# Kernel tuning notes

Measured on AMD Instinct MI355X. Metric: run time of the kernel, lower is better.

## Reference

```python
import jax, jax.numpy as jnp
import numpy as np

TOP_K = 2
HORIZON = 10


def _lstm_layer(seq, w_ih, w_hh, b_ih, b_hh):
    """Single torch-style LSTM layer over seq [T, in]; returns hidden seq [T, hid]."""
    hid = w_hh.shape[1]
    def step(carry, x_t):
        h, c = carry
        z = x_t @ w_ih.T + h @ w_hh.T + b_ih + b_hh  # [4*hid], torch gate order i,f,g,o
        i, f, g, o = jnp.split(z, 4)
        c = jax.nn.sigmoid(f) * c + jax.nn.sigmoid(i) * jnp.tanh(g)
        h = jax.nn.sigmoid(o) * jnp.tanh(c)
        return (h, c), h
    init = (jnp.zeros((hid,), seq.dtype), jnp.zeros((hid,), seq.dtype))
    _, hs = jax.lax.scan(step, init, seq)
    return hs


def setup_inputs() -> dict:
    key = jax.random.key(0)
    ks = jax.random.split(key, 12)
    H, E = 4096, 64
    B, S = 4, 4096
    s = 0.02
    return {
        "x": jax.random.normal(ks[0], (B, S, H), jnp.float32),
        "gate_w": jax.random.normal(ks[1], (E, H), jnp.float32) * s,
        "expert_bias": jnp.zeros((E,), jnp.float32),
        "cp_w1": jax.random.normal(ks[2], (64, H), jnp.float32) * s,
        "cp_b1": jnp.zeros((64,), jnp.float32),
        "cp_w2": jax.random.normal(ks[3], (1, 64), jnp.float32) * s,
        "cp_b2": jnp.zeros((1,), jnp.float32),
        "load_buffer": jax.random.uniform(ks[4], (50, E), jnp.float32),
        "lp_w_ih0": jax.random.normal(ks[5], (256, E), jnp.float32) * s,
        "lp_w_hh0": jax.random.normal(ks[6], (256, 64), jnp.float32) * s,
        "lp_b_ih0": jnp.zeros((256,), jnp.float32),
        "lp_b_hh0": jnp.zeros((256,), jnp.float32),
        "lp_w_ih1": jax.random.normal(ks[7], (256, 64), jnp.float32) * s,
        "lp_w_hh1": jax.random.normal(ks[8], (256, 64), jnp.float32) * s,
        "lp_b_ih1": jnp.zeros((256,), jnp.float32),
        "lp_b_hh1": jnp.zeros((256,), jnp.float32),
        "head_w": jax.random.normal(ks[9], (E * HORIZON, 64), jnp.float32) * s,
        "head_b": jnp.zeros((E * HORIZON,), jnp.float32),
    }


def reference(x, gate_w, expert_bias, cp_w1, cp_b1, cp_w2, cp_b2, load_buffer,
              lp_w_ih0, lp_w_hh0, lp_b_ih0, lp_b_hh0,
              lp_w_ih1, lp_w_hh1, lp_b_ih1, lp_b_hh1, head_w, head_b):
    sg = jax.lax.stop_gradient
    B, S, H = x.shape
    E = gate_w.shape[0]
    flat = x.reshape(-1, H)                       # [N, H]
    N = flat.shape[0]

    # --- routing logits (small gate GEMM) ---
    logits = flat @ gate_w.T                      # [N, E]

    # --- LSTM load prediction (torch.no_grad in original) ---
    seq = sg(load_buffer)
    h1 = _lstm_layer(seq, sg(lp_w_ih0), sg(lp_w_hh0), sg(lp_b_ih0), sg(lp_b_hh0))
    h2 = _lstm_layer(h1, sg(lp_w_ih1), sg(lp_w_hh1), sg(lp_b_ih1), sg(lp_b_hh1))
    pred = h2[-1] @ sg(head_w).T + sg(head_b)     # [E*HORIZON]
    future_load = jax.nn.softmax(pred.reshape(E, HORIZON).mean(axis=1))  # [E]

    # --- bias + predicted-load adjustment, softmax, top-k ---
    adj_logits = logits + expert_bias - sg(future_load)
    probs = jax.nn.softmax(adj_logits, axis=-1)   # [N, E]
    top_scores, top_idx = jax.lax.top_k(probs, TOP_K)
    top_scores = top_scores / top_scores.sum(axis=-1, keepdims=True)

    # --- switch-style load-balancing auxiliary loss ---
    one_hot = jax.nn.one_hot(top_idx, E, dtype=probs.dtype)   # [N, k, E]
    f = one_hot.sum(axis=(0, 1)) / (N * TOP_K)                # routed fraction per expert
    P = probs.mean(axis=0)                                    # mean routing prob
    aux_loss = E * jnp.sum(f * P)

    # --- dynamic capacity from complexity predictor (torch.no_grad) ---
    comp = jax.nn.sigmoid(
        jax.nn.relu(flat @ sg(cp_w1).T + sg(cp_b1)) @ sg(cp_w2).T + sg(cp_b2))  # [N,1]
    capacity = jnp.clip(0.5 + 1.5 * comp.mean(), 0.5, 2.0)

    return top_scores, top_idx, aux_loss, capacity, future_load
```

## Files before the change

kernel.cpp:

```cpp
#include <hip/hip_runtime.h>
#include <stdint.h>

#define IMG_OFF_BYTES 80000
#define CHUNK_IMG 16384
#define LOGITS_OFF 680000
#define SLAB 2097152
#define TAU 1e-3f

#define XLOFF 5120
#define BUF_STRIDE 10240

typedef __attribute__((ext_vector_type(8))) short short8v;
typedef __attribute__((ext_vector_type(4))) short short4v;
typedef __attribute__((ext_vector_type(4))) float f32x4;

__device__ __forceinline__ float rlf(float v, int l) {
  return __int_as_float(__builtin_amdgcn_readlane(__float_as_int(v), l));
}
__device__ __forceinline__ float wsum(float v) {
#pragma unroll
  for (int o = 32; o; o >>= 1) v += __shfl_xor(v, o, 64);
  return v;
}
__device__ __forceinline__ float wmax(float v) {
#pragma unroll
  for (int o = 32; o; o >>= 1) v = fmaxf(v, __shfl_xor(v, o, 64));
  return v;
}
__device__ __forceinline__ unsigned short f2bf(float f) {
  unsigned u = __float_as_uint(f);
  u += 0x7fffu + ((u >> 16) & 1u);
  return (unsigned short)(u >> 16);
}
__device__ __forceinline__ float bf2f(unsigned short h) {
  return __uint_as_float(((unsigned)h) << 16);
}
__device__ __forceinline__ short8v frag8(const char* p0, const char* p1) {
  short4v a = *(const short4v*)p0;
  short4v b = *(const short4v*)p1;
  return __builtin_shufflevector(a, b, 0, 1, 2, 3, 4, 5, 6, 7);
}

__device__ __forceinline__ void lds_barrier() {
  asm volatile("s_waitcnt lgkmcnt(0)" ::: "memory");
  __builtin_amdgcn_s_barrier();
  asm volatile("" ::: "memory");
  __builtin_amdgcn_sched_barrier(0);
}

__global__ __launch_bounds__(256) void prep_kernel(
    const float* __restrict__ gate_w, const float* __restrict__ cp_w1,
    float* __restrict__ ws)
{
  const int c = blockIdx.x;
  const int tid = threadIdx.x;
  if (c == 0 && tid < 144) ws[64 + tid] = 0.f;
  const int row = tid >> 1;
  const int half = tid & 1;
  const float* src = ((row < 64) ? (gate_w + (size_t)row * 4096)
                                 : (cp_w1 + (size_t)(row - 64) * 4096)) + c * 32 + half * 16;
  float v[16];
#pragma unroll
  for (int j = 0; j < 4; ++j) *(float4*)&v[j * 4] = *(const float4*)(src + j * 4);
  const int g = row >> 4, r15 = row & 15;
  char* img = (char*)ws + IMG_OFF_BYTES + (size_t)c * CHUNK_IMG + g * 2048;
#pragma unroll
  for (int q = 0; q < 4; ++q) {
    unsigned short h0 = f2bf(v[4 * q + 0]), h1 = f2bf(v[4 * q + 1]);
    unsigned short h2 = f2bf(v[4 * q + 2]), h3 = f2bf(v[4 * q + 3]);
    unsigned short l0 = f2bf(v[4 * q + 0] - bf2f(h0));
    unsigned short l1 = f2bf(v[4 * q + 1] - bf2f(h1));
    unsigned short l2 = f2bf(v[4 * q + 2] - bf2f(h2));
    unsigned short l3 = f2bf(v[4 * q + 3] - bf2f(h3));
    uint2 hv, lv;
    hv.x = (unsigned)h0 | ((unsigned)h1 << 16);
    hv.y = (unsigned)h2 | ((unsigned)h3 << 16);
    lv.x = (unsigned)l0 | ((unsigned)l1 << 16);
    lv.y = (unsigned)l2 | ((unsigned)l3 << 16);
    const int l = q * 16 + r15;
    *(uint2*)(img + l * 16 + half * 8) = hv;
    *(uint2*)(img + 1024 + l * 16 + half * 8) = lv;
  }
}

__device__ void lstm_device(
    char* ldsbase,
    const float* __restrict__ lb,
    const float* __restrict__ wih0, const float* __restrict__ whh0,
    const float* __restrict__ bih0, const float* __restrict__ bhh0,
    const float* __restrict__ wih1, const float* __restrict__ whh1,
    const float* __restrict__ bih1, const float* __restrict__ bhh1,
    const float* __restrict__ head_w, const float* __restrict__ head_b,
    float* __restrict__ ws, float* __restrict__ out, int N)
{
  float* seqh = (float*)ldsbase;
  float* h1s  = seqh + 3200;
  float* zbuf = h1s + 3200;
  float* hbuf = zbuf + 256;
  float* preds = hbuf + 64;
  const int tid = threadIdx.x;
  const int lane = tid & 63;
  for (int i = tid; i < 3200; i += 256) seqh[i] = lb[i];

  float hv = 0.f;
#pragma unroll 1
  for (int L = 0; L < 2; ++L) {
    const float* wip  = L ? wih1 : wih0;
    const float* whp  = L ? whh1 : whh0;
    const float* bip  = L ? bih1 : bih0;
    const float* bhp  = L ? bhh1 : bhh0;
    const float* seqp = L ? h1s  : seqh;
    float wiR[64], whR[64];
#pragma unroll
    for (int j = 0; j < 64; j += 4) {
      *(float4*)&wiR[j] = *(const float4*)(wip + tid * 64 + j);
      *(float4*)&whR[j] = *(const float4*)(whp + tid * 64 + j);
    }
    const float bsum = bip[tid] + bhp[tid];
    float c_reg = 0.f;
    hv = 0.f;
    if (tid < 64) hbuf[tid] = 0.f;
    __syncthreads();
#pragma unroll 1
    for (int t = 0; t < 50; ++t) {
      const float xv = seqp[t * 64 + lane];
      float a0 = bsum, a1 = 0.f, a2 = 0.f, a3 = 0.f;
#pragma unroll
      for (int j = 0; j < 64; j += 4) {
        a0 = fmaf(rlf(xv, j + 0), wiR[j + 0], a0);
        a1 = fmaf(rlf(xv, j + 1), wiR[j + 1], a1);
        a2 = fmaf(rlf(xv, j + 2), wiR[j + 2], a2);
        a3 = fmaf(rlf(xv, j + 3), wiR[j + 3], a3);
      }
#pragma unroll
      for (int j = 0; j < 64; j += 4) {
        a0 = fmaf(rlf(hv, j + 0), whR[j + 0], a0);
        a1 = fmaf(rlf(hv, j + 1), whR[j + 1], a1);
        a2 = fmaf(rlf(hv, j + 2), whR[j + 2], a2);
        a3 = fmaf(rlf(hv, j + 3), whR[j + 3], a3);
      }
      zbuf[tid] = (a0 + a1) + (a2 + a3);
      __syncthreads();
      if (tid < 64) {
        const float zi = zbuf[tid], zf = zbuf[64 + tid];
        const float zg = zbuf[128 + tid], zo = zbuf[192 + tid];
        const float si = 1.f / (1.f + expf(-zi));
        const float sf = 1.f / (1.f + expf(-zf));
        const float so = 1.f / (1.f + expf(-zo));
        c_reg = sf * c_reg + si * tanhf(zg);
        const float h = so * tanhf(c_reg);
        hbuf[tid] = h;
        if (L == 0) h1s[t * 64 + tid] = h;
      }
      __syncthreads();
      hv = hbuf[lane];
    }
    __syncthreads();
  }
  for (int o = tid; o < 640; o += 256) {
    const float* hw = head_w + o * 64;
    float a0 = 0.f, a1 = 0.f, a2 = 0.f, a3 = 0.f;
#pragma unroll
    for (int j = 0; j < 64; j += 4) {
      a0 = fmaf(rlf(hv, j + 0), hw[j + 0], a0);
      a1 = fmaf(rlf(hv, j + 1), hw[j + 1], a1);
      a2 = fmaf(rlf(hv, j + 2), hw[j + 2], a2);
      a3 = fmaf(rlf(hv, j + 3), hw[j + 3], a3);
    }
    preds[o] = (a0 + a1) + (a2 + a3) + head_b[o];
  }
  __syncthreads();
  if (tid < 64) {
    float m = 0.f;
#pragma unroll
    for (int h = 0; h < 10; ++h) m += preds[tid * 10 + h];
    m = m / 10.f;
    const float mx = wmax(m);
    const float p = expf(m - mx);
    const float s = wsum(p);
    const float flv = p / s;
    ws[tid] = flv;
    out[4 * N + 2 + tid] = flv;
  }
}

__global__ __launch_bounds__(256) void gemm_kernel(
    const float* __restrict__ x, float* __restrict__ ws, float* __restrict__ out,
    const float* __restrict__ lb,
    const float* __restrict__ wih0, const float* __restrict__ whh0,
    const float* __restrict__ bih0, const float* __restrict__ bhh0,
    const float* __restrict__ wih1, const float* __restrict__ whh1,
    const float* __restrict__ bih1, const float* __restrict__ bhh1,
    const float* __restrict__ head_w, const float* __restrict__ head_b,
    int N)
{
  __shared__ __align__(16) char lds[34048];
  if (blockIdx.x == 0) {
    lstm_device(lds, lb, wih0, whh0, bih0, bhh0, wih1, whh1, bih1, bhh1,
                head_w, head_b, ws, out, N);
    return;
  }
  const int b = blockIdx.x - 1;
  const int tb = (b & 255) * 64;
  const int kq = b >> 8;
  const int ck0 = kq * 32;
  const int tid = threadIdx.x;
  const int lane = tid & 63;
  const int wv = __builtin_amdgcn_readfirstlane(tid >> 6);
  const int r15 = lane & 15;
  const int fo = (lane >> 4) * 8;
  const int row = tid >> 2;
  const int kslot = tid & 3;
  const float* xsrc = x + (size_t)(tb + row) * 4096 + kslot * 8;
  const char* wimg = (const char*)ws + IMG_OFF_BYTES;
  char* buf0 = lds;
  char* buf1 = lds + BUF_STRIDE;

  f32x4 acc[4][2];
#pragma unroll
  for (int mi = 0; mi < 4; ++mi)
#pragma unroll
    for (int ni = 0; ni < 2; ++ni) acc[mi][ni] = (f32x4)0.f;

  float xa[8], xb[8];
  short8v whA[2], wlA[2], whB[2], wlB[2];

#define LOADX(R, C)                                                        \
  { *(float4*)&R[0] = *(const float4*)(xsrc + (size_t)(C) * 32);           \
    *(float4*)&R[4] = *(const float4*)(xsrc + (size_t)(C) * 32 + 4); }

#define WRITEX(R, BASE)                                                    \
  { uint4 hv, lv; unsigned hu[4], lu[4];                                   \
    _Pragma("unroll")                                                      \
    for (int i = 0; i < 4; ++i) {                                          \
      unsigned short h0 = f2bf(R[2 * i]), h1 = f2bf(R[2 * i + 1]);         \
      unsigned short l0 = f2bf(R[2 * i] - bf2f(h0));                       \
      unsigned short l1 = f2bf(R[2 * i + 1] - bf2f(h1));                   \
      hu[i] = (unsigned)h0 | ((unsigned)h1 << 16);                         \
      lu[i] = (unsigned)l0 | ((unsigned)l1 << 16);                         \
    }                                                                      \
    hv.x = hu[0]; hv.y = hu[1]; hv.z = hu[2]; hv.w = hu[3];                \
    lv.x = lu[0]; lv.y = lu[1]; lv.z = lu[2]; lv.w = lu[3];                \
    *(uint4*)((BASE) + row * 80 + kslot * 16) = hv;                        \
    *(uint4*)((BASE) + XLOFF + row * 80 + kslot * 16) = lv; }

#define WLOADR(C, WH, WL)                                                  \
  { const char* wb = wimg + (size_t)(C) * CHUNK_IMG + wv * 4096 + lane * 16; \
    WH[0] = *(const short8v*)wb;                                           \
    WL[0] = *(const short8v*)(wb + 1024);                                  \
    WH[1] = *(const short8v*)(wb + 2048);                                  \
    WL[1] = *(const short8v*)(wb + 3072); }

#define COMPUTE(BASE, WH, WL)                                              \
  { short8v xh[4], xl[4];                                                  \
    _Pragma("unroll")                                                      \
    for (int mi = 0; mi < 4; ++mi) {                                       \
      const char* p = (BASE) + (mi * 16 + r15) * 80 + fo;                  \
      xh[mi] = frag8(p, p + 32);                                           \
      xl[mi] = frag8(p + XLOFF, p + XLOFF + 32);                           \
    }                                                                      \
    _Pragma("unroll")                                                      \
    for (int mi = 0; mi < 4; ++mi)                                         \
      _Pragma("unroll")                                                    \
      for (int ni = 0; ni < 2; ++ni) {                                     \
        acc[mi][ni] = __builtin_amdgcn_mfma_f32_16x16x32_bf16(             \
            xh[mi], WH[ni], acc[mi][ni], 0, 0, 0);                         \
        acc[mi][ni] = __builtin_amdgcn_mfma_f32_16x16x32_bf16(             \
            xh[mi], WL[ni], acc[mi][ni], 0, 0, 0);                         \
        acc[mi][ni] = __builtin_amdgcn_mfma_f32_16x16x32_bf16(             \
            xl[mi], WH[ni], acc[mi][ni], 0, 0, 0);                         \
      } }

  LOADX(xa, ck0);
  LOADX(xb, ck0 + 1);
  WLOADR(ck0, whA, wlA);
  WRITEX(xa, buf0);
  lds_barrier();

#pragma unroll 1
  for (int cc = 0; cc < 16; ++cc) {
    const int c0 = ck0 + 2 * cc, c1 = c0 + 1;
    WLOADR(c1, whB, wlB);
    if (cc < 15) LOADX(xa, c0 + 2);
    COMPUTE(buf0, whA, wlA);
    WRITEX(xb, buf1);
    lds_barrier();
    if (cc < 15) WLOADR(c0 + 2, whA, wlA);
    if (cc < 15) LOADX(xb, c1 + 2);
    COMPUTE(buf1, whB, wlB);
    if (cc < 15) WRITEX(xa, buf0);
    lds_barrier();
  }

  float (*souts)[132] = (float(*)[132])lds;
#pragma unroll
  for (int mi = 0; mi < 4; ++mi)
#pragma unroll
    for (int ni = 0; ni < 2; ++ni)
#pragma unroll
      for (int r = 0; r < 4; ++r)
        souts[mi * 16 + (lane >> 4) * 4 + r][wv * 32 + ni * 16 + r15] =
            acc[mi][ni][r];
  lds_barrier();
  {
    float* slab = ws + LOGITS_OFF + (size_t)kq * SLAB;
    const int srow = tid >> 2, sq = tid & 3;
    float4* dst = (float4*)(slab + (size_t)(tb + srow) * 128 + sq * 32);
    const float4* srcp = (const float4*)&souts[srow][sq * 32];
#pragma unroll
    for (int i = 0; i < 8; ++i) dst[i] = srcp[i];
  }
#undef LOADX
#undef WRITEX
#undef WLOADR
#undef COMPUTE
}

__global__ __launch_bounds__(256) void epi_kernel(
    const float* __restrict__ eb_p, const float* __restrict__ cp_b1,
    const float* __restrict__ cp_w2, const float* __restrict__ cp_b2,
    float* __restrict__ ws, float* __restrict__ out, int N)
{
  const int tid = threadIdx.x;
  const int lane = tid & 63;
  const int wv = __builtin_amdgcn_readfirstlane(tid >> 6);
  const int tb = blockIdx.x * 32;
  const float* lg = ws + LOGITS_OFF;
  int* qd = (int*)(ws + 200);
  __shared__ float sP[64];
  __shared__ float scnt[64];
  __shared__ float scomp;
  if (tid < 64) { sP[tid] = 0.f; scnt[tid] = 0.f; }
  if (tid == 0) scomp = 0.f;
  __syncthreads();

  const float eb = eb_p[lane];
  const float fl = ws[lane];
  const float cb1 = cp_b1[lane];
  const float cw2 = cp_w2[lane];
  const float cb2 = cp_b2[0];
  float psum_local = 0.f, comp_local = 0.f;
  float* o_ts = out;
  float* o_ti = out + 2 * N;

#pragma unroll 1
  for (int tt = 0; tt < 8; ++tt) {
    const int tok = tb + wv * 8 + tt;
    const size_t base = (size_t)tok * 128;
    const float lgv = ((lg[base + lane] + lg[SLAB + base + lane]) +
                       (lg[2 * SLAB + base + lane] + lg[3 * SLAB + base + lane]));
    const float lc  = ((lg[base + 64 + lane] + lg[SLAB + base + 64 + lane]) +
                       (lg[2 * SLAB + base + 64 + lane] + lg[3 * SLAB + base + 64 + lane]));
    float rr = fmaxf(lc + cb1, 0.f) * cw2;
    rr = wsum(rr);
    const float comp = 1.f / (1.f + expf(-(rr + cb2)));
    comp_local += comp;
    const float a = lgv + eb - fl;
    float m1 = a; int i1 = lane;
#pragma unroll
    for (int o = 32; o; o >>= 1) {
      const float ov = __shfl_xor(m1, o, 64);
      const int oi = __shfl_xor(i1, o, 64);
      if (ov > m1 || (ov == m1 && oi < i1)) { m1 = ov; i1 = oi; }
    }
    float m2 = (lane == i1) ? -1e30f : a; int i2 = lane;
#pragma unroll
    for (int o = 32; o; o >>= 1) {
      const float ov = __shfl_xor(m2, o, 64);
      const int oi = __shfl_xor(i2, o, 64);
      if (ov > m2 || (ov == m2 && oi < i2)) { m2 = ov; i2 = oi; }
    }
    float m3 = (lane == i1 || lane == i2) ? -1e30f : a;
#pragma unroll
    for (int o = 32; o; o >>= 1) m3 = fmaxf(m3, __shfl_xor(m3, o, 64));
    const float p = expf(a - m1);
    const float ssum = wsum(p);
    const float prob = p / ssum;
    psum_local += prob;
    const float s1 = rlf(prob, i1);
    const float s2 = rlf(prob, i2);
    if (lane == 0) {
      const float inv = 1.f / (s1 + s2);
      o_ts[tok * 2 + 0] = s1 * inv;
      o_ts[tok * 2 + 1] = s2 * inv;
      o_ti[tok * 2 + 0] = (float)i1;
      o_ti[tok * 2 + 1] = (float)i2;
      atomicAdd(&scnt[i1], 1.f);
      atomicAdd(&scnt[i2], 1.f);
      if (m1 - m2 < TAU || m2 - m3 < TAU) {
        int slot = atomicAdd(qd, 1);
        qd[8 + slot] = tok;
      }
    }
  }
  atomicAdd(&sP[lane], psum_local);
  if (lane == 0) atomicAdd(&scomp, comp_local);
  __syncthreads();
  if (tid < 64) {
    atomicAdd(&ws[64 + tid], sP[tid]);
    atomicAdd(&ws[128 + tid], scnt[tid]);
  }
  if (tid == 0) atomicAdd(&ws[192], scomp);
}

__global__ __launch_bounds__(256) void repair_kernel(
    const float* __restrict__ x, const float* __restrict__ gate_w,
    const float* __restrict__ eb_p, float* __restrict__ ws,
    float* __restrict__ out, int N)
{
  const int tid = threadIdx.x;
  __shared__ float red[256];
  int* qd = (int*)(ws + 200);
  const int qn = qd[0];
  float* o_ts = out;
  float* o_ti = out + 2 * N;

  for (int e = blockIdx.x; e < qn; e += gridDim.x) {
    const int tok = qd[8 + e];
    const int o = tid & 63;
    const int kq = tid >> 6;
    const float* xr = x + (size_t)tok * 4096 + kq * 1024;
    const float* wr = gate_w + (size_t)o * 4096 + kq * 1024;
    float s = 0.f;
#pragma unroll 4
    for (int j = 0; j < 256; ++j) {
      const float4 xv = *(const float4*)(xr + j * 4);
      const float4 wv = *(const float4*)(wr + j * 4);
      s = fmaf(xv.x, wv.x, s); s = fmaf(xv.y, wv.y, s);
      s = fmaf(xv.z, wv.z, s); s = fmaf(xv.w, wv.w, s);
    }
    red[tid] = s;
    __syncthreads();
    if (tid < 64) {
      const float a = red[tid] + red[64 + tid] + red[128 + tid] +
                      red[192 + tid] + eb_p[tid] - ws[tid];
      const int lane = tid;
      float m1 = a; int i1 = lane;
#pragma unroll
      for (int oo = 32; oo; oo >>= 1) {
        const float ov = __shfl_xor(m1, oo, 64);
        const int oi = __shfl_xor(i1, oo, 64);
        if (ov > m1 || (ov == m1 && oi < i1)) { m1 = ov; i1 = oi; }
      }
      float m2 = (lane == i1) ? -1e30f : a; int i2 = lane;
#pragma unroll
      for (int oo = 32; oo; oo >>= 1) {
        const float ov = __shfl_xor(m2, oo, 64);
        const int oi = __shfl_xor(i2, oo, 64);
        if (ov > m2 || (ov == m2 && oi < i2)) { m2 = ov; i2 = oi; }
      }
      const float p = expf(a - m1);
      const float ssum = wsum(p);
      const float s1 = rlf(p, i1) / ssum;
      const float s2 = rlf(p, i2) / ssum;
      if (lane == 0) {
        const int i1o = (int)o_ti[tok * 2 + 0];
        const int i2o = (int)o_ti[tok * 2 + 1];
        const float inv = 1.f / (s1 + s2);
        o_ts[tok * 2 + 0] = s1 * inv;
        o_ts[tok * 2 + 1] = s2 * inv;
        o_ti[tok * 2 + 0] = (float)i1;
        o_ti[tok * 2 + 1] = (float)i2;
        if (i1o != i1 || i2o != i2) {
          atomicAdd(&ws[128 + i1o], -1.f);
          atomicAdd(&ws[128 + i2o], -1.f);
          atomicAdd(&ws[128 + i1], 1.f);
          atomicAdd(&ws[128 + i2], 1.f);
        }
      }
    }
    __syncthreads();
  }
}

__global__ __launch_bounds__(64) void fin_kernel(const float* __restrict__ ws,
                                                 float* __restrict__ out, int N) {
  const int e = threadIdx.x;
  const float P = ws[64 + e] / (float)N;
  const float f = ws[128 + e] / (float)(2 * N);
  const float v = wsum(f * P);
  if (e == 0) {
    out[4 * N + 0] = 64.f * v;
    float cap = 0.5f + 1.5f * (ws[192] / (float)N);
    out[4 * N + 1] = fminf(fmaxf(cap, 0.5f), 2.f);
  }
}

extern "C" void kernel_launch(void* const* d_in, const int* in_sizes, int n_in,
                              void* d_out, int out_size, void* d_ws, size_t ws_size,
                              hipStream_t stream) {
  const float* x          = (const float*)d_in[0];
  const float* gate_w     = (const float*)d_in[1];
  const float* expert_bias= (const float*)d_in[2];
  const float* cp_w1      = (const float*)d_in[3];
  const float* cp_b1      = (const float*)d_in[4];
  const float* cp_w2      = (const float*)d_in[5];
  const float* cp_b2      = (const float*)d_in[6];
  const float* load_buffer= (const float*)d_in[7];
  const float* wih0       = (const float*)d_in[8];
  const float* whh0       = (const float*)d_in[9];
  const float* bih0       = (const float*)d_in[10];
  const float* bhh0       = (const float*)d_in[11];
  const float* wih1       = (const float*)d_in[12];
  const float* whh1       = (const float*)d_in[13];
  const float* bih1       = (const float*)d_in[14];
  const float* bhh1       = (const float*)d_in[15];
  const float* head_w     = (const float*)d_in[16];
  const float* head_b     = (const float*)d_in[17];
  float* out = (float*)d_out;
  float* ws  = (float*)d_ws;
  const int N = in_sizes[0] / 4096;

  prep_kernel<<<128, 256, 0, stream>>>(gate_w, cp_w1, ws);
  gemm_kernel<<<1025, 256, 0, stream>>>(x, ws, out, load_buffer,
                                        wih0, whh0, bih0, bhh0,
                                        wih1, whh1, bih1, bhh1,
                                        head_w, head_b, N);
  epi_kernel<<<N / 32, 256, 0, stream>>>(expert_bias, cp_b1, cp_w2, cp_b2,
                                         ws, out, N);
  repair_kernel<<<128, 256, 0, stream>>>(x, gate_w, expert_bias, ws, out, N);
  fin_kernel<<<1, 64, 0, stream>>>(ws, out, N);
}
```

Measured before the change: 216.6 us.

## Load x straight into registers as MFMA fragments, dropping LDS staging and barriers

The GEMM kernel no longer stages x through double-buffered LDS with barriers. Each wave now loads its own 32 token rows directly from global memory into registers and splits them into bf16 hi/lo MFMA operands in place. Weight fragments are streamed from the prepacked image one group at a time, interleaved with the MFMAs. Tiles grow to 128 tokens per block with half as many blocks, and results are stored straight to the logits slab without an LDS transpose. This removes LDS traffic and synchronisation, but increases register pressure (16 accumulators) and each wave now reloads the weights on its own.

Result: slower. 287.7 us (+32.8%).

```diff
diff --git a/kernel.cpp b/kernel.cpp
--- a/kernel.cpp
+++ b/kernel.cpp
@@ -7,12 +7,9 @@
 #define SLAB 2097152
 #define TAU 1e-3f
 
-#define XLOFF 5120
-#define BUF_STRIDE 10240
-
 typedef __attribute__((ext_vector_type(8))) short short8v;
-typedef __attribute__((ext_vector_type(4))) short short4v;
 typedef __attribute__((ext_vector_type(4))) float f32x4;
+typedef unsigned short ushort;
 
 __device__ __forceinline__ float rlf(float v, int l) {
   return __int_as_float(__builtin_amdgcn_readlane(__float_as_int(v), l));
@@ -27,25 +24,30 @@
   for (int o = 32; o; o >>= 1) v = fmaxf(v, __shfl_xor(v, o, 64));
   return v;
 }
-__device__ __forceinline__ unsigned short f2bf(float f) {
+__device__ __forceinline__ ushort f2bf(float f) {
   unsigned u = __float_as_uint(f);
   u += 0x7fffu + ((u >> 16) & 1u);
-  return (unsigned short)(u >> 16);
-}
-__device__ __forceinline__ float bf2f(unsigned short h) {
+  return (ushort)(u >> 16);
+}
+__device__ __forceinline__ float bf2f(ushort h) {
   return __uint_as_float(((unsigned)h) << 16);
 }
-__device__ __forceinline__ short8v frag8(const char* p0, const char* p1) {
-  short4v a = *(const short4v*)p0;
-  short4v b = *(const short4v*)p1;
-  return __builtin_shufflevector(a, b, 0, 1, 2, 3, 4, 5, 6, 7);
-}
-
-__device__ __forceinline__ void lds_barrier() {
-  asm volatile("s_waitcnt lgkmcnt(0)" ::: "memory");
-  __builtin_amdgcn_s_barrier();
-  asm volatile("" ::: "memory");
-  __builtin_amdgcn_sched_barrier(0);
+
+__device__ __forceinline__ void split8(const float4 a, const float4 b,
+                                       short8v& hv, short8v& lv) {
+  union { ushort u[8]; short8v v; } H, L;
+  const float f[8] = {a.x, a.y, a.z, a.w, b.x, b.y, b.z, b.w};
+#pragma unroll
+  for (int i = 0; i < 8; ++i) {
+    unsigned u = __float_as_uint(f[i]);
+    unsigned t = u + 0x7fffu + ((u >> 16) & 1u);
+    H.u[i] = (ushort)(t >> 16);
+    const float e = f[i] - __uint_as_float(t & 0xffff0000u);
+    unsigned ue = __float_as_uint(e);
+    unsigned te = ue + 0x7fffu + ((ue >> 16) & 1u);
+    L.u[i] = (ushort)(te >> 16);
+  }
+  hv = H.v; lv = L.v;
 }
 
 __global__ __launch_bounds__(256) void prep_kernel(
@@ -66,12 +68,12 @@
   char* img = (char*)ws + IMG_OFF_BYTES + (size_t)c * CHUNK_IMG + g * 2048;
 #pragma unroll
   for (int q = 0; q < 4; ++q) {
-    unsigned short h0 = f2bf(v[4 * q + 0]), h1 = f2bf(v[4 * q + 1]);
-    unsigned short h2 = f2bf(v[4 * q + 2]), h3 = f2bf(v[4 * q + 3]);
-    unsigned short l0 = f2bf(v[4 * q + 0] - bf2f(h0));
-    unsigned short l1 = f2bf(v[4 * q + 1] - bf2f(h1));
-    unsigned short l2 = f2bf(v[4 * q + 2] - bf2f(h2));
-    unsigned short l3 = f2bf(v[4 * q + 3] - bf2f(h3));
+    ushort h0 = f2bf(v[4 * q + 0]), h1 = f2bf(v[4 * q + 1]);
+    ushort h2 = f2bf(v[4 * q + 2]), h3 = f2bf(v[4 * q + 3]);
+    ushort l0 = f2bf(v[4 * q + 0] - bf2f(h0));
+    ushort l1 = f2bf(v[4 * q + 1] - bf2f(h1));
+    ushort l2 = f2bf(v[4 * q + 2] - bf2f(h2));
+    ushort l3 = f2bf(v[4 * q + 3] - bf2f(h3));
     uint2 hv, lv;
     hv.x = (unsigned)h0 | ((unsigned)h1 << 16);
     hv.y = (unsigned)h2 | ((unsigned)h3 << 16);
@@ -194,126 +196,96 @@
     const float* __restrict__ head_w, const float* __restrict__ head_b,
     int N)
 {
-  __shared__ __align__(16) char lds[34048];
+  __shared__ __align__(16) char lds[29440];
   if (blockIdx.x == 0) {
     lstm_device(lds, lb, wih0, whh0, bih0, bhh0, wih1, whh1, bih1, bhh1,
                 head_w, head_b, ws, out, N);
     return;
   }
   const int b = blockIdx.x - 1;
-  const int tb = (b & 255) * 64;
-  const int kq = b >> 8;
+  const int tile = (b & 127) * 128;
+  const int kq = b >> 7;
   const int ck0 = kq * 32;
-  const int tid = threadIdx.x;
-  const int lane = tid & 63;
-  const int wv = __builtin_amdgcn_readfirstlane(tid >> 6);
+  const int lane = threadIdx.x & 63;
+  const int wv = __builtin_amdgcn_readfirstlane(threadIdx.x >> 6);
   const int r15 = lane & 15;
-  const int fo = (lane >> 4) * 8;
-  const int row = tid >> 2;
-  const int kslot = tid & 3;
-  const float* xsrc = x + (size_t)(tb + row) * 4096 + kslot * 8;
+  const int q = lane >> 4;
+
+  const float* xs0 = x + (size_t)(tile + wv * 32 + r15) * 4096 + ck0 * 32 + q * 4;
+  const float* xs1 = xs0 + (size_t)16 * 4096;
   const char* wimg = (const char*)ws + IMG_OFF_BYTES;
-  char* buf0 = lds;
-  char* buf1 = lds + BUF_STRIDE;
-
-  f32x4 acc[4][2];
-#pragma unroll
-  for (int mi = 0; mi < 4; ++mi)
-#pragma unroll
-    for (int ni = 0; ni < 2; ++ni) acc[mi][ni] = (f32x4)0.f;
-
-  float xa[8], xb[8];
-  short8v whA[2], wlA[2], whB[2], wlB[2];
-
-#define LOADX(R, C)                                                        \
-  { *(float4*)&R[0] = *(const float4*)(xsrc + (size_t)(C) * 32);           \
-    *(float4*)&R[4] = *(const float4*)(xsrc + (size_t)(C) * 32 + 4); }
-
-#define WRITEX(R, BASE)                                                    \
-  { uint4 hv, lv; unsigned hu[4], lu[4];                                   \
-    _Pragma("unroll")                                                      \
-    for (int i = 0; i < 4; ++i) {                                          \
-      unsigned short h0 = f2bf(R[2 * i]), h1 = f2bf(R[2 * i + 1]);         \
-      unsigned short l0 = f2bf(R[2 * i] - bf2f(h0));                       \
-      unsigned short l1 = f2bf(R[2 * i + 1] - bf2f(h1));                   \
-      hu[i] = (unsigned)h0 | ((unsigned)h1 << 16);                         \
-      lu[i] = (unsigned)l0 | ((unsigned)l1 << 16);                         \
-    }                                                                      \
-    hv.x = hu[0]; hv.y = hu[1]; hv.z = hu[2]; hv.w = hu[3];                \
-    lv.x = lu[0]; lv.y = lu[1]; lv.z = lu[2]; lv.w = lu[3];                \
-    *(uint4*)((BASE) + row * 80 + kslot * 16) = hv;                        \
-    *(uint4*)((BASE) + XLOFF + row * 80 + kslot * 16) = lv; }
-
-#define WLOADR(C, WH, WL)                                                  \
-  { const char* wb = wimg + (size_t)(C) * CHUNK_IMG + wv * 4096 + lane * 16; \
-    WH[0] = *(const short8v*)wb;                                           \
-    WL[0] = *(const short8v*)(wb + 1024);                                  \
-    WH[1] = *(const short8v*)(wb + 2048);                                  \
-    WL[1] = *(const short8v*)(wb + 3072); }
-
-#define COMPUTE(BASE, WH, WL)                                              \
-  { short8v xh[4], xl[4];                                                  \
-    _Pragma("unroll")                                                      \
-    for (int mi = 0; mi < 4; ++mi) {                                       \
-      const char* p = (BASE) + (mi * 16 + r15) * 80 + fo;                  \
-      xh[mi] = frag8(p, p + 32);                                           \
-      xl[mi] = frag8(p + XLOFF, p + XLOFF + 32);                           \
-    }                                                                      \
-    _Pragma("unroll")                                                      \
-    for (int mi = 0; mi < 4; ++mi)                                         \
-      _Pragma("unroll")                                                    \
-      for (int ni = 0; ni < 2; ++ni) {                                     \
-        acc[mi][ni] = __builtin_amdgcn_mfma_f32_16x16x32_bf16(             \
-            xh[mi], WH[ni], acc[mi][ni], 0, 0, 0);                         \
-        acc[mi][ni] = __builtin_amdgcn_mfma_f32_16x16x32_bf16(             \
-            xh[mi], WL[ni], acc[mi][ni], 0, 0, 0);                         \
-        acc[mi][ni] = __builtin_amdgcn_mfma_f32_16x16x32_bf16(             \
-            xl[mi], WH[ni], acc[mi][ni], 0, 0, 0);                         \
-      } }
-
-  LOADX(xa, ck0);
-  LOADX(xb, ck0 + 1);
-  WLOADR(ck0, whA, wlA);
-  WRITEX(xa, buf0);
-  lds_barrier();
+
+  f32x4 acc[8][2];
+#pragma unroll
+  for (int g = 0; g < 8; ++g)
+#pragma unroll
+    for (int s = 0; s < 2; ++s) acc[g][s] = (f32x4)0.f;
+
+  float4 raE[2], rbE[2], raO[2], rbO[2];
+  short8v xh[2], xl[2];
+  short8v whA, wlA, whB, wlB;
+
+#define LX(RA, RB, RC)                                                      \
+  { RA[0] = *(const float4*)(xs0 + (RC) * 32);                              \
+    RB[0] = *(const float4*)(xs0 + (RC) * 32 + 16);                         \
+    RA[1] = *(const float4*)(xs1 + (RC) * 32);                              \
+    RB[1] = *(const float4*)(xs1 + (RC) * 32 + 16); }
+
+#define WG(RC, G, WH, WL)                                                   \
+  { const char* p_ = wimg + (size_t)((ck0 + (RC)) & 127) * CHUNK_IMG +      \
+                     (G) * 2048 + lane * 16;                                \
+    WH = *(const short8v*)p_;                                               \
+    WL = *(const short8v*)(p_ + 1024); }
+
+#define M3(G, WH, WL)                                                       \
+  { acc[G][0] = __builtin_amdgcn_mfma_f32_16x16x32_bf16(WH, xh[0], acc[G][0], 0, 0, 0); \
+    acc[G][0] = __builtin_amdgcn_mfma_f32_16x16x32_bf16(WL, xh[0], acc[G][0], 0, 0, 0); \
+    acc[G][0] = __builtin_amdgcn_mfma_f32_16x16x32_bf16(WH, xl[0], acc[G][0], 0, 0, 0); \
+    acc[G][1] = __builtin_amdgcn_mfma_f32_16x16x32_bf16(WH, xh[1], acc[G][1], 0, 0, 0); \
+    acc[G][1] = __builtin_amdgcn_mfma_f32_16x16x32_bf16(WL, xh[1], acc[G][1], 0, 0, 0); \
+    acc[G][1] = __builtin_amdgcn_mfma_f32_16x16x32_bf16(WH, xl[1], acc[G][1], 0, 0, 0); }
+
+#define CHUNK(RC, RA, RB)                                                   \
+  { split8(RA[0], RB[0], xh[0], xl[0]);                                     \
+    split8(RA[1], RB[1], xh[1], xl[1]);                                     \
+    if ((RC) + 2 < 32) LX(RA, RB, (RC) + 2);                                \
+    WG(RC, 1, whB, wlB);  M3(0, whA, wlA);                                  \
+    WG(RC, 2, whA, wlA);  M3(1, whB, wlB);                                  \
+    WG(RC, 3, whB, wlB);  M3(2, whA, wlA);                                  \
+    WG(RC, 4, whA, wlA);  M3(3, whB, wlB);                                  \
+    WG(RC, 5, whB, wlB);  M3(4, whA, wlA);                                  \
+    WG(RC, 6, whA, wlA);  M3(5, whB, wlB);                                  \
+    WG(RC, 7, whB, wlB);  M3(6, whA, wlA);                                  \
+    WG((RC) + 1, 0, whA, wlA);  M3(7, whB, wlB); }
+
+  LX(raE, rbE, 0);
+  LX(raO, rbO, 1);
+  WG(0, 0, whA, wlA);
 
 #pragma unroll 1
-  for (int cc = 0; cc < 16; ++cc) {
-    const int c0 = ck0 + 2 * cc, c1 = c0 + 1;
-    WLOADR(c1, whB, wlB);
-    if (cc < 15) LOADX(xa, c0 + 2);
-    COMPUTE(buf0, whA, wlA);
-    WRITEX(xb, buf1);
-    lds_barrier();
-    if (cc < 15) WLOADR(c0 + 2, whA, wlA);
-    if (cc < 15) LOADX(xb, c1 + 2);
-    COMPUTE(buf1, whB, wlB);
-    if (cc < 15) WRITEX(xa, buf0);
-    lds_barrier();
-  }
-
-  float (*souts)[132] = (float(*)[132])lds;
-#pragma unroll
-  for (int mi = 0; mi < 4; ++mi)
-#pragma unroll
-    for (int ni = 0; ni < 2; ++ni)
-#pragma unroll
-      for (int r = 0; r < 4; ++r)
-        souts[mi * 16 + (lane >> 4) * 4 + r][wv * 32 + ni * 16 + r15] =
-            acc[mi][ni][r];
-  lds_barrier();
+  for (int it = 0; it < 16; ++it) {
+    const int rc = 2 * it;
+    CHUNK(rc, raE, rbE);
+    CHUNK(rc + 1, raO, rbO);
+  }
+
   {
     float* slab = ws + LOGITS_OFF + (size_t)kq * SLAB;
-    const int srow = tid >> 2, sq = tid & 3;
-    float4* dst = (float4*)(slab + (size_t)(tb + srow) * 128 + sq * 32);
-    const float4* srcp = (const float4*)&souts[srow][sq * 32];
-#pragma unroll
-    for (int i = 0; i < 8; ++i) dst[i] = srcp[i];
-  }
-#undef LOADX
-#undef WRITEX
-#undef WLOADR
-#undef COMPUTE
+#pragma unroll
+    for (int g = 0; g < 8; ++g)
+#pragma unroll
+      for (int s = 0; s < 2; ++s) {
+        const int tok = tile + wv * 32 + s * 16 + r15;
+        float4 v;
+        v.x = acc[g][s][0]; v.y = acc[g][s][1];
+        v.z = acc[g][s][2]; v.w = acc[g][s][3];
+        *(float4*)(slab + (size_t)tok * 128 + g * 16 + q * 4) = v;
+      }
+  }
+#undef LX
+#undef WG
+#undef M3
+#undef CHUNK
 }
 
 __global__ __launch_bounds__(256) void epi_kernel(
@@ -512,10 +484,10 @@
   const int N = in_sizes[0] / 4096;
 
   prep_kernel<<<128, 256, 0, stream>>>(gate_w, cp_w1, ws);
-  gemm_kernel<<<1025, 256, 0, stream>>>(x, ws, out, load_buffer,
-                                        wih0, whh0, bih0, bhh0,
-                                        wih1, whh1, bih1, bhh1,
-                                        head_w, head_b, N);
+  gemm_kernel<<<513, 256, 0, stream>>>(x, ws, out, load_buffer,
+                                       wih0, whh0, bih0, bhh0,
+                                       wih1, whh1, bih1, bhh1,
+                                       head_w, head_b, N);
   epi_kernel<<<N / 32, 256, 0, stream>>>(expert_bias, cp_b1, cp_w2, cp_b2,
                                          ws, out, N);
   repair_kernel<<<128, 256, 0, stream>>>(x, gate_w, expert_bias, ws, out, N);
```

## Split LSTM predictor out of GEMM kernel into its own launch

Applied to the files above, without the earlier changes.

Moves the single-block LSTM load predictor out of block 0 of the GEMM kernel into a dedicated kernel launched before prep and GEMM. This removes the LSTM's large register footprint (two 64-float weight arrays per thread) and its branch from the GEMM kernel, which may improve GEMM register allocation and occupancy. In exchange, the long sequential LSTM recurrence now runs alone on one block in stream order. It is no longer hidden behind the GEMM's blocks, which adds its latency to the critical path.

Measured after the change: 281.7 us. 1.3x slower.

```diff
diff --git a/kernel.cpp b/kernel.cpp
--- a/kernel.cpp
+++ b/kernel.cpp
@@ -46,6 +46,107 @@
   __builtin_amdgcn_s_barrier();
   asm volatile("" ::: "memory");
   __builtin_amdgcn_sched_barrier(0);
+}
+
+__global__ __launch_bounds__(256) void lstm_kernel(
+    const float* __restrict__ lb,
+    const float* __restrict__ wih0, const float* __restrict__ whh0,
+    const float* __restrict__ bih0, const float* __restrict__ bhh0,
+    const float* __restrict__ wih1, const float* __restrict__ whh1,
+    const float* __restrict__ bih1, const float* __restrict__ bhh1,
+    const float* __restrict__ head_w, const float* __restrict__ head_b,
+    float* __restrict__ ws, float* __restrict__ out, int N)
+{
+  const int tid = threadIdx.x;
+  const int lane = tid & 63;
+  __shared__ float seqh[50 * 64];
+  __shared__ float h1s[50 * 64];
+  __shared__ float zbuf[256];
+  __shared__ float hbuf[64];
+  __shared__ float preds[640];
+
+  for (int i = tid; i < 3200; i += 256) seqh[i] = lb[i];
+
+  float hv = 0.f;
+#pragma unroll 1
+  for (int L = 0; L < 2; ++L) {
+    const float* wip  = L ? wih1 : wih0;
+    const float* whp  = L ? whh1 : whh0;
+    const float* bip  = L ? bih1 : bih0;
+    const float* bhp  = L ? bhh1 : bhh0;
+    const float* seqp = L ? h1s  : seqh;
+    float wiR[64], whR[64];
+#pragma unroll
+    for (int j = 0; j < 64; j += 4) {
+      *(float4*)&wiR[j] = *(const float4*)(wip + tid * 64 + j);
+      *(float4*)&whR[j] = *(const float4*)(whp + tid * 64 + j);
+    }
+    const float bsum = bip[tid] + bhp[tid];
+    float c_reg = 0.f;
+    hv = 0.f;
+    if (tid < 64) hbuf[tid] = 0.f;
+    __syncthreads();
+#pragma unroll 1
+    for (int t = 0; t < 50; ++t) {
+      const float xv = seqp[t * 64 + lane];
+      float a0 = bsum, a1 = 0.f, a2 = 0.f, a3 = 0.f;
+#pragma unroll
+      for (int j = 0; j < 64; j += 4) {
+        a0 = fmaf(rlf(xv, j + 0), wiR[j + 0], a0);
+        a1 = fmaf(rlf(xv, j + 1), wiR[j + 1], a1);
+        a2 = fmaf(rlf(xv, j + 2), wiR[j + 2], a2);
+        a3 = fmaf(rlf(xv, j + 3), wiR[j + 3], a3);
+      }
+#pragma unroll
+      for (int j = 0; j < 64; j += 4) {
+        a0 = fmaf(rlf(hv, j + 0), whR[j + 0], a0);
+        a1 = fmaf(rlf(hv, j + 1), whR[j + 1], a1);
+        a2 = fmaf(rlf(hv, j + 2), whR[j + 2], a2);
+        a3 = fmaf(rlf(hv, j + 3), whR[j + 3], a3);
+      }
+      zbuf[tid] = (a0 + a1) + (a2 + a3);
+      __syncthreads();
+      if (tid < 64) {
+        const float zi = zbuf[tid], zf = zbuf[64 + tid];
+        const float zg = zbuf[128 + tid], zo = zbuf[192 + tid];
+        const float si = 1.f / (1.f + expf(-zi));
+        const float sf = 1.f / (1.f + expf(-zf));
+        const float so = 1.f / (1.f + expf(-zo));
+        c_reg = sf * c_reg + si * tanhf(zg);
+        const float h = so * tanhf(c_reg);
+        hbuf[tid] = h;
+        if (L == 0) h1s[t * 64 + tid] = h;
+      }
+      __syncthreads();
+      hv = hbuf[lane];
+    }
+    __syncthreads();
+  }
+  for (int o = tid; o < 640; o += 256) {
+    const float* hw = head_w + o * 64;
+    float a0 = 0.f, a1 = 0.f, a2 = 0.f, a3 = 0.f;
+#pragma unroll
+    for (int j = 0; j < 64; j += 4) {
+      a0 = fmaf(rlf(hv, j + 0), hw[j + 0], a0);
+      a1 = fmaf(rlf(hv, j + 1), hw[j + 1], a1);
+      a2 = fmaf(rlf(hv, j + 2), hw[j + 2], a2);
+      a3 = fmaf(rlf(hv, j + 3), hw[j + 3], a3);
+    }
+    preds[o] = (a0 + a1) + (a2 + a3) + head_b[o];
+  }
+  __syncthreads();
+  if (tid < 64) {
+    float m = 0.f;
+#pragma unroll
+    for (int h = 0; h < 10; ++h) m += preds[tid * 10 + h];
+    m = m / 10.f;
+    const float mx = wmax(m);
+    const float p = expf(m - mx);
+    const float s = wsum(p);
+    const float flv = p / s;
+    ws[tid] = flv;
+    out[4 * N + 2 + tid] = flv;
+  }
 }
 
 __global__ __launch_bounds__(256) void prep_kernel(
@@ -83,124 +184,11 @@
   }
 }
 
-__device__ void lstm_device(
-    char* ldsbase,
-    const float* __restrict__ lb,
-    const float* __restrict__ wih0, const float* __restrict__ whh0,
-    const float* __restrict__ bih0, const float* __restrict__ bhh0,
-    const float* __restrict__ wih1, const float* __restrict__ whh1,
-    const float* __restrict__ bih1, const float* __restrict__ bhh1,
-    const float* __restrict__ head_w, const float* __restrict__ head_b,
-    float* __restrict__ ws, float* __restrict__ out, int N)
-{
-  float* seqh = (float*)ldsbase;
-  float* h1s  = seqh + 3200;
-  float* zbuf = h1s + 3200;
-  float* hbuf = zbuf + 256;
-  float* preds = hbuf + 64;
-  const int tid = threadIdx.x;
-  const int lane = tid & 63;
-  for (int i = tid; i < 3200; i += 256) seqh[i] = lb[i];
-
-  float hv = 0.f;
-#pragma unroll 1
-  for (int L = 0; L < 2; ++L) {
-    const float* wip  = L ? wih1 : wih0;
-    const float* whp  = L ? whh1 : whh0;
-    const float* bip  = L ? bih1 : bih0;
-    const float* bhp  = L ? bhh1 : bhh0;
-    const float* seqp = L ? h1s  : seqh;
-    float wiR[64], whR[64];
-#pragma unroll
-    for (int j = 0; j < 64; j += 4) {
-      *(float4*)&wiR[j] = *(const float4*)(wip + tid * 64 + j);
-      *(float4*)&whR[j] = *(const float4*)(whp + tid * 64 + j);
-    }
-    const float bsum = bip[tid] + bhp[tid];
-    float c_reg = 0.f;
-    hv = 0.f;
-    if (tid < 64) hbuf[tid] = 0.f;
-    __syncthreads();
-#pragma unroll 1
-    for (int t = 0; t < 50; ++t) {
-      const float xv = seqp[t * 64 + lane];
-      float a0 = bsum, a1 = 0.f, a2 = 0.f, a3 = 0.f;
-#pragma unroll
-      for (int j = 0; j < 64; j += 4) {
-        a0 = fmaf(rlf(xv, j + 0), wiR[j + 0], a0);
-        a1 = fmaf(rlf(xv, j + 1), wiR[j + 1], a1);
-        a2 = fmaf(rlf(xv, j + 2), wiR[j + 2], a2);
-        a3 = fmaf(rlf(xv, j + 3), wiR[j + 3], a3);
-      }
-#pragma unroll
-      for (int j = 0; j < 64; j += 4) {
-        a0 = fmaf(rlf(hv, j + 0), whR[j + 0], a0);
-        a1 = fmaf(rlf(hv, j + 1), whR[j + 1], a1);
-        a2 = fmaf(rlf(hv, j + 2), whR[j + 2], a2);
-        a3 = fmaf(rlf(hv, j + 3), whR[j + 3], a3);
-      }
-      zbuf[tid] = (a0 + a1) + (a2 + a3);
-      __syncthreads();
-      if (tid < 64) {
-        const float zi = zbuf[tid], zf = zbuf[64 + tid];
-        const float zg = zbuf[128 + tid], zo = zbuf[192 + tid];
-        const float si = 1.f / (1.f + expf(-zi));
-        const float sf = 1.f / (1.f + expf(-zf));
-        const float so = 1.f / (1.f + expf(-zo));
-        c_reg = sf * c_reg + si * tanhf(zg);
-        const float h = so * tanhf(c_reg);
-        hbuf[tid] = h;
-        if (L == 0) h1s[t * 64 + tid] = h;
-      }
-      __syncthreads();
-      hv = hbuf[lane];
-    }
-    __syncthreads();
-  }
-  for (int o = tid; o < 640; o += 256) {
-    const float* hw = head_w + o * 64;
-    float a0 = 0.f, a1 = 0.f, a2 = 0.f, a3 = 0.f;
-#pragma unroll
-    for (int j = 0; j < 64; j += 4) {
-      a0 = fmaf(rlf(hv, j + 0), hw[j + 0], a0);
-      a1 = fmaf(rlf(hv, j + 1), hw[j + 1], a1);
-      a2 = fmaf(rlf(hv, j + 2), hw[j + 2], a2);
-      a3 = fmaf(rlf(hv, j + 3), hw[j + 3], a3);
-    }
-    preds[o] = (a0 + a1) + (a2 + a3) + head_b[o];
-  }
-  __syncthreads();
-  if (tid < 64) {
-    float m = 0.f;
-#pragma unroll
-    for (int h = 0; h < 10; ++h) m += preds[tid * 10 + h];
-    m = m / 10.f;
-    const float mx = wmax(m);
-    const float p = expf(m - mx);
-    const float s = wsum(p);
-    const float flv = p / s;
-    ws[tid] = flv;
-    out[4 * N + 2 + tid] = flv;
-  }
-}
-
 __global__ __launch_bounds__(256) void gemm_kernel(
-    const float* __restrict__ x, float* __restrict__ ws, float* __restrict__ out,
-    const float* __restrict__ lb,
-    const float* __restrict__ wih0, const float* __restrict__ whh0,
-    const float* __restrict__ bih0, const float* __restrict__ bhh0,
-    const float* __restrict__ wih1, const float* __restrict__ whh1,
-    const float* __restrict__ bih1, const float* __restrict__ bhh1,
-    const float* __restrict__ head_w, const float* __restrict__ head_b,
-    int N)
+    const float* __restrict__ x, float* __restrict__ ws, int N)
 {
   __shared__ __align__(16) char lds[34048];
-  if (blockIdx.x == 0) {
-    lstm_device(lds, lb, wih0, whh0, bih0, bhh0, wih1, whh1, bih1, bhh1,
-                head_w, head_b, ws, out, N);
-    return;
-  }
-  const int b = blockIdx.x - 1;
+  const int b = blockIdx.x;
   const int tb = (b & 255) * 64;
   const int kq = b >> 8;
   const int ck0 = kq * 32;
@@ -511,11 +499,11 @@
   float* ws  = (float*)d_ws;
   const int N = in_sizes[0] / 4096;
 
+  lstm_kernel<<<1, 256, 0, stream>>>(load_buffer, wih0, whh0, bih0, bhh0,
+                                     wih1, whh1, bih1, bhh1, head_w, head_b,
+                                     ws, out, N);
   prep_kernel<<<128, 256, 0, stream>>>(gate_w, cp_w1, ws);
-  gemm_kernel<<<1025, 256, 0, stream>>>(x, ws, out, load_buffer,
-                                        wih0, whh0, bih0, bhh0,
-                                        wih1, whh1, bih1, bhh1,
-                                        head_w, head_b, N);
+  gemm_kernel<<<1024, 256, 0, stream>>>(x, ws, N);
   epi_kernel<<<N / 32, 256, 0, stream>>>(expert_bias, cp_b1, cp_w2, cp_b2,
                                          ws, out, N);
   repair_kernel<<<128, 256, 0, stream>>>(x, gate_w, expert_bias, ws, out, N);
```
